# Kernel tuning notes

Hardware: AMD Instinct MI355X
Metric: run time of the kernel (lower is better)

## Reference

```python
import jax, jax.numpy as jnp
import numpy as np

K = 40  # neighbors, self.k = 40 in the module
BN_EPS = 1e-5


def knn(x, k):
    # x: (B, C, N) -> indices of k nearest points (largest negative sq-dist)
    xx = jnp.sum(x * x, axis=1, keepdims=True)            # (B, 1, N)
    inner = -2.0 * jnp.einsum('bcn,bcm->bnm', x, x)       # (B, N, N)
    pd = -xx - inner - jnp.swapaxes(xx, 1, 2)             # (B, N, N) = -||xi-xj||^2
    _, idx = jax.lax.top_k(pd, k)                         # (B, N, k)
    return idx


def graph_cov(x, k):
    # Faithful port of get_graph_dynamic_covariance (dim9=False, idx=None)
    B, C, N = x.shape
    idx = knn(x, k)                                       # (B, N, k)
    xt = jnp.swapaxes(x, 1, 2)                            # (B, N, C)
    feature = xt[jnp.arange(B)[:, None, None], idx]       # gather: (B, N, k, C)
    xc = xt[:, :, None, :]                                # (B, N, 1, C)
    rel = feature - xc                                    # relative positions
    var = jnp.var(rel, axis=2, ddof=1)                    # torch.var is unbiased
    relf = rel * (1.0 - var)[:, :, None, :]
    relf = jnp.concatenate([jnp.broadcast_to(xc, rel.shape), relf], axis=3)
    norm = rel - jnp.mean(rel, axis=0)                    # mean over BATCH dim, as in source
    cov = jnp.einsum('bnkc,bnjc->bnkj', rel, norm)        # (B, N, k, k)
    out = jnp.concatenate([relf, cov], axis=3)            # (B, N, k, 2C+k)
    return jnp.transpose(out, (0, 3, 1, 2))               # (B, 2C+k, N, k)


def bn(x, g, b):
    # train-mode BatchNorm (batch statistics, biased variance), eps=1e-5
    axes = (0,) + tuple(range(2, x.ndim))
    m = jnp.mean(x, axis=axes, keepdims=True)
    v = jnp.var(x, axis=axes, keepdims=True)
    shp = (1, -1) + (1,) * (x.ndim - 2)
    return g.reshape(shp) * (x - m) * jax.lax.rsqrt(v + BN_EPS) + b.reshape(shp)


def blk(x, W, g, b):
    # Conv(1x1, no bias) + BN + LeakyReLU(0.2)
    return jax.nn.leaky_relu(bn(jnp.einsum('oi,bi...->bo...', W, x), g, b), 0.2)


def forward(x, l, W3, W4, W5, W6, W7, W8, W9, W10, W11, W12,
            g3, b3, g4, b4, g5, b5, g6, b6, g7, b7, g8, b8, g9, b9,
            g10, b10, g11, b11):
    B, _, N = x.shape
    rc = blk(blk(graph_cov(x, K), W3, g3, b3), W4, g4, b4)       # (B,64,N,K)
    rc_ = jnp.max(rc, axis=-1)                                    # (B,64,N)
    drc = blk(blk(graph_cov(rc_, K), W5, g5, b5), W6, g6, b6)
    drc_ = jnp.max(drc, axis=-1)                                  # (B,64,N)
    allf = jnp.concatenate([rc_, drc_], axis=1)                   # (B,128,N)
    h = jnp.max(blk(allf, W7, g7, b7), axis=-1, keepdims=True)    # (B,1024,1)
    lv = blk(l.reshape(B, -1, 1), W8, g8, b8)                     # (B,64,1)
    h = jnp.concatenate([h, lv], axis=1)                          # (B,1088,1)
    h = jnp.broadcast_to(h, (B, h.shape[1], N))
    h = jnp.concatenate([h, rc_, drc_], axis=1)                   # (B,1216,N)
    h = blk(h, W9, g9, b9)
    h = blk(h, W10, g10, b10)                                     # dropout is eval-mode identity
    h = blk(h, W11, g11, b11)
    return jnp.einsum('oi,bin->bon', W12, h)                      # (B,50,N)


def setup_inputs():
    key = jax.random.key(0)
    ks = jax.random.split(key, 12)
    B, N = 4, 2048
    d = {}
    d['x'] = jax.random.normal(ks[0], (B, 3, N), jnp.float32)
    lab = jax.random.randint(ks[1], (B,), 0, 16)
    d['l'] = jax.nn.one_hot(lab, 16, dtype=jnp.float32)
    wdims = {'W3': (64, 46), 'W4': (64, 64), 'W5': (64, 168), 'W6': (64, 64),
             'W7': (1024, 128), 'W8': (64, 16), 'W9': (512, 1216),
             'W10': (256, 512), 'W11': (128, 256), 'W12': (50, 128)}
    for i, (name, shp) in enumerate(wdims.items()):
        d[name] = jax.random.normal(ks[2 + i], shp, jnp.float32) / np.float32(np.sqrt(shp[1]))
    for name, c in [('g3', 64), ('g4', 64), ('g5', 64), ('g6', 64), ('g7', 1024),
                    ('g8', 64), ('g9', 512), ('g10', 256), ('g11', 128)]:
        d[name] = jnp.ones((c,), jnp.float32)
        d['b' + name[1:]] = jnp.zeros((c,), jnp.float32)
    return d


def reference(x, l, W3, W4, W5, W6, W7, W8, W9, W10, W11, W12,
              g3, b3, g4, b4, g5, b5, g6, b6, g7, b7, g8, b8, g9, b9,
              g10, b10, g11, b11):
    return forward(x, l, W3, W4, W5, W6, W7, W8, W9, W10, W11, W12,
                   g3, b3, g4, b4, g5, b5, g6, b6, g7, b7, g8, b8, g9, b9,
                   g10, b10, g11, b11)
```

## Files before the change

### kernel.cpp

```cpp
#include <hip/hip_runtime.h>
#include <math.h>

#define NB 4
#define NP 2048
#define KNN 40
#define BEPS 1e-5f
#define NSLOT 64
#define CMCH 16

typedef unsigned long long u64;

static __device__ __forceinline__ float leaky(float x) { return x >= 0.f ? x : 0.2f * x; }

static __device__ __forceinline__ u64 keyOf(float v, int m) {
  unsigned u = __float_as_uint(v);
  u ^= (u >> 31) ? 0xFFFFFFFFu : 0x80000000u;
  return ((u64)u << 32) | (unsigned)(NP - 1 - m);
}
static __device__ __forceinline__ u64 umax64(u64 a, u64 b) { return a > b ? a : b; }

static __device__ __forceinline__ void select40_dual(float (*pd)[NP], int* __restrict__ out0,
                                                     int* __restrict__ out1, int tid,
                                                     u64* red, u64* red2, int* sh_w) {
  int h = tid >> 7, t = tid & 127;
  int* outp = h ? out1 : out0;
  u64 myBest = 0;
  #pragma unroll
  for (int j = 0; j < 16; ++j) myBest = umax64(myBest, keyOf(pd[h][t + j*128], t + j*128));
  for (int kk = 0; kk < KNN; ++kk) {
    red[tid] = myBest;
    __syncthreads();
    if (t < 16) {
      u64 v = red[h*128 + t];
      #pragma unroll
      for (int j = 1; j < 8; ++j) v = umax64(v, red[h*128 + t + j*16]);
      red2[h*16 + t] = v;
    }
    __syncthreads();
    if (t == 0) {
      u64 v = red2[h*16];
      #pragma unroll
      for (int j = 1; j < 16; ++j) v = umax64(v, red2[h*16 + j]);
      int w = NP - 1 - (int)(v & 0xFFFFFFFFu);
      outp[kk] = w;
      pd[h][w] = -INFINITY;
      sh_w[h] = w;
    }
    __syncthreads();
    if ((sh_w[h] & 127) == t) {
      u64 nb = 0;
      #pragma unroll
      for (int j = 0; j < 16; ++j) nb = umax64(nb, keyOf(pd[h][t + j*128], t + j*128));
      myBest = nb;
    }
  }
}

__global__ __launch_bounds__(256) void canary_kernel(float* __restrict__ out, int n, float val) {
  int i = blockIdx.x*256 + threadIdx.x;
  if (i < n) out[i] = val;
}

__global__ __launch_bounds__(256) void knn3_kernel(const float* __restrict__ x, int* __restrict__ idx) {
  int b = blockIdx.y, n0 = blockIdx.x*2, tid = threadIdx.x;
  __shared__ float pd[2][NP];
  __shared__ float xq[2][3];
  __shared__ float xxq[2];
  __shared__ u64 red[256];
  __shared__ u64 red2[32];
  __shared__ int sh_w[2];
  if (tid < 2) {
    int n = n0 + tid;
    float a0 = x[(b*3+0)*NP+n], a1 = x[(b*3+1)*NP+n], a2 = x[(b*3+2)*NP+n];
    xq[tid][0] = a0; xq[tid][1] = a1; xq[tid][2] = a2;
    xxq[tid] = __fadd_rn(__fadd_rn(__fmul_rn(a0,a0), __fmul_rn(a1,a1)), __fmul_rn(a2,a2));
  }
  __syncthreads();
  for (int m = tid; m < NP; m += 256) {
    float m0 = x[(b*3+0)*NP+m], m1 = x[(b*3+1)*NP+m], m2 = x[(b*3+2)*NP+m];
    float xxm = __fadd_rn(__fadd_rn(__fmul_rn(m0,m0), __fmul_rn(m1,m1)), __fmul_rn(m2,m2));
    #pragma unroll
    for (int q = 0; q < 2; ++q) {
      float dot = __fmaf_rn(xq[q][2], m2, __fmaf_rn(xq[q][1], m1, __fmul_rn(xq[q][0], m0)));
      float inner = __fmul_rn(-2.f, dot);
      pd[q][m] = __fsub_rn(__fsub_rn(-xxm, inner), xxq[q]);
    }
  }
  __syncthreads();
  select40_dual(pd, &idx[((size_t)b*NP + n0)*KNN], &idx[((size_t)b*NP + n0 + 1)*KNN], tid, red, red2, sh_w);
}

__global__ __launch_bounds__(256) void xx64_kernel(const float* __restrict__ rc, float* __restrict__ xx) {
  int i = blockIdx.x*256 + threadIdx.x;
  if (i >= NB*NP) return;
  const float* p = &rc[(size_t)i*64];
  float s = __fmul_rn(p[0], p[0]);
  #pragma unroll
  for (int c = 1; c < 64; ++c) s = __fadd_rn(s, __fmul_rn(p[c], p[c]));
  xx[i] = s;
}

__global__ __launch_bounds__(256) void knn64_kernel(const float* __restrict__ rc, const float* __restrict__ xx,
                                                    int* __restrict__ idx) {
  int b = blockIdx.y, n0 = blockIdx.x*2, tid = threadIdx.x;
  __shared__ float pd[2][NP];
  __shared__ float xn[2][64];
  __shared__ u64 red[256];
  __shared__ u64 red2[32];
  __shared__ int sh_w[2];
  if (tid < 128) xn[tid >> 6][tid & 63] = rc[((size_t)b*NP + n0 + (tid >> 6))*64 + (tid & 63)];
  __syncthreads();
  float xxn0 = xx[b*NP + n0], xxn1 = xx[b*NP + n0 + 1];
  for (int m = tid; m < NP; m += 256) {
    const float* xm = &rc[((size_t)b*NP + m)*64];
    float v0 = xm[0];
    float d0 = __fmul_rn(xn[0][0], v0);
    float d1 = __fmul_rn(xn[1][0], v0);
    #pragma unroll
    for (int c = 1; c < 64; ++c) {
      float v = xm[c];
      d0 = __fmaf_rn(xn[0][c], v, d0);
      d1 = __fmaf_rn(xn[1][c], v, d1);
    }
    float xxm = xx[b*NP + m];
    pd[0][m] = __fsub_rn(__fsub_rn(-xxm, __fmul_rn(-2.f, d0)), xxn0);
    pd[1][m] = __fsub_rn(__fsub_rn(-xxm, __fmul_rn(-2.f, d1)), xxn1);
  }
  __syncthreads();
  select40_dual(pd, &idx[((size_t)b*NP + n0)*KNN], &idx[((size_t)b*NP + n0 + 1)*KNN], tid, red, red2, sh_w);
}


__global__ __launch_bounds__(256) void s1a_kernel(
    const float* __restrict__ x, const int* __restrict__ idx1, const float* __restrict__ W3,
    double* __restrict__ stslots, float* __restrict__ y)
{
  int b = blockIdx.y, n = blockIdx.x, tid = threadIdx.x;
  __shared__ int sidx[4][KNN];
  __shared__ float rs[KNN][4];
  __shared__ float ns[KNN][4];
  __shared__ float scale[3];
  __shared__ __align__(16) float feat[KNN*48];
  __shared__ float w3s[64*48];
  __shared__ double sred[4][64];

  for (int i = tid; i < 4*KNN; i += 256) sidx[i/KNN][i%KNN] = idx1[((i/KNN)*NP + n)*KNN + (i%KNN)];
  for (int i = tid; i < 64*48; i += 256) { int o = i/48, ci = i%48; w3s[i] = (ci < 46) ? W3[o*46+ci] : 0.f; }
  __syncthreads();
  for (int i = tid; i < KNN*3; i += 256) {
    int k = i/3, c = i%3;
    float ctr = x[(b*3+c)*NP + n];
    float r = x[(b*3+c)*NP + sidx[b][k]] - ctr;
    float s = 0.f;
    for (int b2 = 0; b2 < 4; ++b2) s += x[(b2*3+c)*NP + sidx[b2][k]] - x[(b2*3+c)*NP + n];
    rs[k][c] = r; ns[k][c] = r - 0.25f*s;
  }
  __syncthreads();
  if (tid < 3) {
    float s = 0.f; for (int k = 0; k < KNN; ++k) s += rs[k][tid];
    float m = s/(float)KNN; float v = 0.f;
    for (int k = 0; k < KNN; ++k) { float d = rs[k][tid]-m; v += d*d; }
    scale[tid] = 1.f - v/(float)(KNN-1);
  }
  __syncthreads();
  for (int i = tid; i < KNN*48; i += 256) {
    int k = i/48, ci = i%48; float v;
    if (ci < 3) v = x[(b*3+ci)*NP+n];
    else if (ci < 6) v = rs[k][ci-3]*scale[ci-3];
    else if (ci < 46) { int j = ci-6; v = rs[k][0]*ns[j][0] + rs[k][1]*ns[j][1] + rs[k][2]*ns[j][2]; }
    else v = 0.f;
    feat[i] = v;
  }
  __syncthreads();

  int o = tid & 63, kg = tid >> 6;
  float acc[10];
  #pragma unroll
  for (int t = 0; t < 10; ++t) acc[t] = 0.f;
  for (int ci4 = 0; ci4 < 12; ++ci4) {
    float w0 = w3s[o*48+ci4*4+0], w1 = w3s[o*48+ci4*4+1], w2 = w3s[o*48+ci4*4+2], w3c = w3s[o*48+ci4*4+3];
    #pragma unroll
    for (int t = 0; t < 10; ++t) {
      float4 f4 = *(const float4*)&feat[(kg*10+t)*48 + ci4*4];
      acc[t] += f4.x*w0 + f4.y*w1 + f4.z*w2 + f4.w*w3c;
    }
  }
  size_t bn40 = (size_t)(b*NP+n)*KNN;
  #pragma unroll
  for (int t = 0; t < 10; ++t) y[(bn40 + kg*10+t)*64 + o] = acc[t];
  double s = 0.0, s2 = 0.0;
  #pragma unroll
  for (int t = 0; t < 10; ++t) { double a = acc[t]; s += a; s2 += a*a; }
  int slot = (blockIdx.y*NP + blockIdx.x) & (NSLOT-1);
  sred[kg][o] = s; __syncthreads();
  if (kg == 0) atomicAdd(&stslots[slot*128 + o], sred[0][o]+sred[1][o]+sred[2][o]+sred[3][o]);
  __syncthreads();
  sred[kg][o] = s2; __syncthreads();
  if (kg == 0) atomicAdd(&stslots[slot*128 + 64 + o], sred[0][o]+sred[1][o]+sred[2][o]+sred[3][o]);
}

__global__ __launch_bounds__(256) void s2a_kernel(
    const float* __restrict__ rc, const int* __restrict__ idx2, const float* __restrict__ W5,
    double* __restrict__ stslots, float* __restrict__ y)
{
  int b = blockIdx.y, n = blockIdx.x, tid = threadIdx.x;
  __shared__ int sidx[4][KNN];
  __shared__ float rsT[64*41];
  __shared__ float nsT[64*41];
  __shared__ float scale[64];
  __shared__ __align__(16) float feat[KNN*168];
  __shared__ double sred[4][64];

  for (int i = tid; i < 4*KNN; i += 256) sidx[i/KNN][i%KNN] = idx2[((i/KNN)*NP + n)*KNN + (i%KNN)];
  __syncthreads();
  for (int i = tid; i < KNN*64; i += 256) {
    int k = i >> 6, c = i & 63;
    float ctr = rc[((size_t)(b*NP+n))*64 + c];
    float r = rc[((size_t)(b*NP) + sidx[b][k])*64 + c] - ctr;
    float s = 0.f;
    for (int b2 = 0; b2 < 4; ++b2)
      s += rc[((size_t)(b2*NP) + sidx[b2][k])*64 + c] - rc[((size_t)(b2*NP+n))*64 + c];
    rsT[c*41+k] = r; nsT[c*41+k] = r - 0.25f*s;
  }
  __syncthreads();
  if (tid < 64) {
    int c = tid;
    float s = 0.f; for (int k = 0; k < KNN; ++k) s += rsT[c*41+k];
    float m = s/(float)KNN; float v = 0.f;
    for (int k = 0; k < KNN; ++k) { float d = rsT[c*41+k]-m; v += d*d; }
    scale[c] = 1.f - v/(float)(KNN-1);
  }
  __syncthreads();
  for (int i = tid; i < KNN*128; i += 256) {
    int k = i >> 7, ci = i & 127;
    float v;
    if (ci < 64) v = rc[((size_t)(b*NP+n))*64 + ci];
    else v = rsT[(ci-64)*41 + k]*scale[ci-64];
    feat[k*168 + ci] = v;
  }
  for (int p = tid; p < KNN*KNN; p += 256) {
    int k = p/KNN, j = p%KNN;
    float acc = __fmul_rn(rsT[k], nsT[j]);
    #pragma unroll 8
    for (int c = 1; c < 64; ++c) acc = __fmaf_rn(rsT[c*41+k], nsT[c*41+j], acc);
    feat[k*168 + 128 + j] = acc;
  }
  __syncthreads();

  int o = tid & 63, kg = tid >> 6;
  float acc[10];
  #pragma unroll
  for (int t = 0; t < 10; ++t) acc[t] = 0.f;
  for (int ci4 = 0; ci4 < 42; ++ci4) {
    float4 wv = *(const float4*)&W5[(size_t)o*168 + ci4*4];
    #pragma unroll
    for (int t = 0; t < 10; ++t) {
      float4 f4 = *(const float4*)&feat[(kg*10+t)*168 + ci4*4];
      acc[t] += f4.x*wv.x + f4.y*wv.y + f4.z*wv.z + f4.w*wv.w;
    }
  }
  size_t bn40 = (size_t)(b*NP+n)*KNN;
  #pragma unroll
  for (int t = 0; t < 10; ++t) y[(bn40 + kg*10+t)*64 + o] = acc[t];
  double s = 0.0, s2 = 0.0;
  #pragma unroll
  for (int t = 0; t < 10; ++t) { double a = acc[t]; s += a; s2 += a*a; }
  int slot = (blockIdx.y*NP + blockIdx.x) & (NSLOT-1);
  sred[kg][o] = s; __syncthreads();
  if (kg == 0) atomicAdd(&stslots[slot*128 + o], sred[0][o]+sred[1][o]+sred[2][o]+sred[3][o]);
  __syncthreads();
  sred[kg][o] = s2; __syncthreads();
  if (kg == 0) atomicAdd(&stslots[slot*128 + 64 + o], sred[0][o]+sred[1][o]+sred[2][o]+sred[3][o]);
}

__global__ __launch_bounds__(256) void mid_kernel(
    float* __restrict__ y, const float* __restrict__ W,
    const double* __restrict__ stp, const float* __restrict__ gv, const float* __restrict__ bv,
    double* __restrict__ stslots)
{
  int b = blockIdx.y, n = blockIdx.x, tid = threadIdx.x;
  __shared__ float m_s[64], sc_s[64], bo_s[64];
  __shared__ __align__(16) float ytile[KNN*68];
  __shared__ double sred[4][64];
  const double INV_M1 = 1.0/327680.0;

  if (tid < 64) {
    double md = stp[tid]*INV_M1;
    double vd = stp[64+tid]*INV_M1 - md*md;
    m_s[tid] = (float)md;
    sc_s[tid] = gv[tid]/sqrtf((float)vd + BEPS);
    bo_s[tid] = bv[tid];
  }
  __syncthreads();
  size_t bn40 = (size_t)(b*NP+n)*KNN;
  for (int i = tid; i < KNN*64; i += 256) {
    int k = i >> 6, c = i & 63;
    float v = y[(bn40 + k)*64 + c];
    ytile[k*68+c] = leaky(sc_s[c]*(v - m_s[c]) + bo_s[c]);
  }
  __syncthreads();
  int o = tid & 63, kg = tid >> 6;
  float acc2[10];
  #pragma unroll
  for (int t = 0; t < 10; ++t) acc2[t] = 0.f;
  for (int c4 = 0; c4 < 16; ++c4) {
    float4 wv = *(const float4*)&W[(size_t)o*64 + c4*4];
    #pragma unroll
    for (int t = 0; t < 10; ++t) {
      float4 y4 = *(const float4*)&ytile[(kg*10+t)*68 + c4*4];
      acc2[t] += y4.x*wv.x + y4.y*wv.y + y4.z*wv.z + y4.w*wv.w;
    }
  }
  #pragma unroll
  for (int t = 0; t < 10; ++t) y[(bn40 + kg*10+t)*64 + o] = acc2[t];
  double s = 0.0, s2 = 0.0;
  #pragma unroll
  for (int t = 0; t < 10; ++t) { double a = acc2[t]; s += a; s2 += a*a; }
  int slot = (blockIdx.y*NP + blockIdx.x) & (NSLOT-1);
  sred[kg][o] = s; __syncthreads();
  if (kg == 0) atomicAdd(&stslots[slot*128 + o], sred[0][o]+sred[1][o]+sred[2][o]+sred[3][o]);
  __syncthreads();
  sred[kg][o] = s2; __syncthreads();
  if (kg == 0) atomicAdd(&stslots[slot*128 + 64 + o], sred[0][o]+sred[1][o]+sred[2][o]+sred[3][o]);
}

__global__ __launch_bounds__(256) void maxk_bn_kernel(
    const float* __restrict__ y, const double* __restrict__ stp,
    const float* __restrict__ gv, const float* __restrict__ bv, float* __restrict__ out)
{
  int i = blockIdx.x*256 + threadIdx.x;
  if (i >= NB*NP*64) return;
  int o = i & 63; int bn = i >> 6;
  const double INV_M1 = 1.0/327680.0;
  double md = stp[o]*INV_M1;
  double vd = stp[64+o]*INV_M1 - md*md;
  float m = (float)md;
  float sc = gv[o]/sqrtf((float)vd + BEPS);
  float bo = bv[o];
  float mx = -INFINITY;
  size_t base = (size_t)bn*KNN;
  for (int k = 0; k < KNN; ++k) {
    float v = y[(base + k)*64 + o];
    mx = fmaxf(mx, leaky(sc*(v-m) + bo));
  }
  out[(size_t)bn*64 + o] = mx;
}

__global__ __launch_bounds__(128) void redstats_kernel(const double* __restrict__ slots, double* __restrict__ st) {
  int c = threadIdx.x;
  double s = 0.0;
  for (int i = 0; i < NSLOT; ++i) s += slots[i*128 + c];
  st[c] = s;
}

__global__ __launch_bounds__(256) void allf_kernel(const float* __restrict__ rc, const float* __restrict__ drc,
                                                   float* __restrict__ out) {
  int i = blockIdx.x*256 + threadIdx.x;
  if (i >= NB*NP*128) return;
  int c = i & 127; int bn = i >> 7;
  out[i] = (c < 64) ? rc[(size_t)bn*64 + c] : drc[(size_t)bn*64 + (c-64)];
}

#define GBM 64
#define GBN 64
#define GBK 16
__global__ __launch_bounds__(256) void gemm_kernel(const float* __restrict__ A, const float* __restrict__ W,
                                                   float* __restrict__ C, int M, int No, int Kd,
                                                   int wstride, int woff, const float* __restrict__ bias) {
  __shared__ __align__(16) float As[GBK][GBM+8];
  __shared__ __align__(16) float Ws[GBK][GBN+8];
  int bm = blockIdx.y * GBM, bn = blockIdx.x * GBN;
  int tid = threadIdx.x;
  int tx = tid % 16, ty = tid / 16;
  float acc[4][4] = {{0.f}};
  for (int k0 = 0; k0 < Kd; k0 += GBK) {
    for (int i = tid; i < GBM*GBK; i += 256) {
      int r = i / GBK, c = i % GBK;
      int gm = bm + r, gk = k0 + c;
      As[c][r] = (gk < Kd && gm < M) ? A[(size_t)gm*Kd + gk] : 0.f;
      int gn = bn + r;
      Ws[c][r] = (gk < Kd && gn < No) ? W[(size_t)gn*wstride + woff + gk] : 0.f;
    }
    __syncthreads();
    #pragma unroll
    for (int kk = 0; kk < GBK; ++kk) {
      float4 a4 = *(const float4*)&As[kk][ty*4];
      float4 w4 = *(const float4*)&Ws[kk][tx*4];
      float av[4] = {a4.x, a4.y, a4.z, a4.w};
      float wv[4] = {w4.x, w4.y, w4.z, w4.w};
      #pragma unroll
      for (int i2 = 0; i2 < 4; ++i2)
        #pragma unroll
        for (int j2 = 0; j2 < 4; ++j2)
          acc[i2][j2] += av[i2]*wv[j2];
    }
    __syncthreads();
  }
  for (int i2 = 0; i2 < 4; ++i2) {
    int gm = bm + ty*4 + i2;
    if (gm >= M) continue;
    for (int j2 = 0; j2 < 4; ++j2) {
      int gn = bn + tx*4 + j2;
      if (gn < No) {
        float v = acc[i2][j2];
        if (bias) v += bias[(gm >> 11)*No + gn];
        C[(size_t)gm*No + gn] = v;
      }
    }
  }
}

__global__ __launch_bounds__(256) void colstats_kernel(const float* __restrict__ A, long M, int C,
                                                       int rowsPerBlock, double* __restrict__ st) {
  long r0 = (long)blockIdx.x * rowsPerBlock;
  long r1 = r0 + rowsPerBlock; if (r1 > M) r1 = M;
  int tid = threadIdx.x;
  if (C >= 256) {
    for (int c0 = 0; c0 < C; c0 += 256) {
      int c = c0 + tid;
      double s = 0.0, s2 = 0.0;
      for (long r = r0; r < r1; ++r) { double v = A[r*(long)C + c]; s += v; s2 += v*v; }
      atomicAdd(&st[c], s); atomicAdd(&st[C+c], s2);
    }
  } else {
    int c = tid % C; int grp = tid / C; int G = 256 / C;
    double s = 0.0, s2 = 0.0;
    for (long r = r0 + grp; r < r1; r += G) { double v = A[r*(long)C + c]; s += v; s2 += v*v; }
    __shared__ double sh[512];
    sh[tid] = s; sh[256+tid] = s2; __syncthreads();
    for (int g = G/2; g > 0; g >>= 1) {
      if (grp < g) { sh[tid] += sh[tid + g*C]; sh[256+tid] += sh[256+tid + g*C]; }
      __syncthreads();
    }
    if (grp == 0) { atomicAdd(&st[c], sh[tid]); atomicAdd(&st[C+c], sh[256+tid]); }
  }
}

__global__ __launch_bounds__(256) void bnapply_kernel(float* __restrict__ A, const double* __restrict__ st,
                                                      const float* __restrict__ g, const float* __restrict__ bb,
                                                      double invM, int cmask, size_t total) {
  size_t i = (size_t)blockIdx.x*256 + threadIdx.x;
  if (i >= total) return;
  int c = (int)(i & cmask);
  int C = cmask + 1;
  double md = st[c]*invM;
  double vd = st[C+c]*invM - md*md;
  float m = (float)md;
  float sc = g[c]/sqrtf((float)vd + BEPS);
  float y = sc*(A[i]-m) + bb[c];
  A[i] = leaky(y);
}

__global__ __launch_bounds__(256) void colmax_part_kernel(const float* __restrict__ A, int C,
                                                          float* __restrict__ pmax) {
  int i = blockIdx.x*256 + threadIdx.x;
  if (i >= NB*CMCH*C) return;
  int c = i % C; int t = i / C; int ch = t % CMCH; int b = t / CMCH;
  int n0 = ch * (NP/CMCH);
  float mx = -INFINITY;
  for (int n = n0; n < n0 + NP/CMCH; ++n)
    mx = fmaxf(mx, A[((size_t)(b*NP+n))*C + c]);
  pmax[(size_t)(b*CMCH+ch)*C + c] = mx;
}
__global__ __launch_bounds__(256) void colmax_fin_kernel(const float* __restrict__ pmax, int C,
                                                         float* __restrict__ out) {
  int i = blockIdx.x*256 + threadIdx.x;
  if (i >= NB*C) return;
  int b = i / C, c = i % C;
  float mx = -INFINITY;
  for (int ch = 0; ch < CMCH; ++ch) mx = fmaxf(mx, pmax[(size_t)(b*CMCH+ch)*C + c]);
  out[i] = mx;
}

__global__ __launch_bounds__(256) void lv_kernel(const float* __restrict__ l, const float* __restrict__ W8,
                                                 const float* __restrict__ g8, const float* __restrict__ b8,
                                                 float* __restrict__ lv) {
  __shared__ float raw[4][64];
  int tid = threadIdx.x;
  {
    int b = tid / 64, o = tid % 64;
    float s = 0.f;
    for (int i = 0; i < 16; ++i) s += W8[o*16+i]*l[b*16+i];
    raw[b][o] = s;
  }
  __syncthreads();
  if (tid < 64) {
    int o = tid;
    float m = (raw[0][o]+raw[1][o]+raw[2][o]+raw[3][o])*0.25f;
    float v = 0.f;
    for (int b = 0; b < 4; ++b) { float d = raw[b][o]-m; v += d*d; }
    v *= 0.25f;
    float sc = g8[o]/sqrtf(v + BEPS);
    for (int b = 0; b < 4; ++b) {
      float y = sc*(raw[b][o]-m) + b8[o];
      lv[b*64+o] = leaky(y);
    }
  }
}

__global__ __launch_bounds__(256) void bias9_kernel(const float* __restrict__ hmax, const float* __restrict__ lv,
                                                    const float* __restrict__ W9, float* __restrict__ bias9) {
  int i = blockIdx.x*256 + threadIdx.x;
  if (i >= 4*512) return;
  int b = i >> 9, o = i & 511;
  const float* wr = &W9[(size_t)o*1216];
  float s = 0.f;
  for (int c = 0; c < 1024; ++c) s += hmax[b*1024+c]*wr[c];
  for (int c = 0; c < 64; ++c) s += lv[b*64+c]*wr[1024+c];
  bias9[i] = s;
}

__global__ __launch_bounds__(256) void out_kernel(const float* __restrict__ h5, float* __restrict__ out) {
  int i = blockIdx.x*256 + threadIdx.x;
  if (i >= NB*50*NP) return;
  int n = i % NP; int t = i / NP; int o = t % 50; int b = t / 50;
  out[i] = h5[((size_t)(b*NP+n))*50 + o];
}

extern "C" void kernel_launch(void* const* d_in, const int* in_sizes, int n_in,
                              void* d_out, int out_size, void* d_ws, size_t ws_size,
                              hipStream_t stream) {
  const float* x   = (const float*)d_in[0];
  const float* l   = (const float*)d_in[1];
  const float* W3  = (const float*)d_in[2];
  const float* W4  = (const float*)d_in[3];
  const float* W5  = (const float*)d_in[4];
  const float* W6  = (const float*)d_in[5];
  const float* W7  = (const float*)d_in[6];
  const float* W8  = (const float*)d_in[7];
  const float* W9  = (const float*)d_in[8];
  const float* W10 = (const float*)d_in[9];
  const float* W11 = (const float*)d_in[10];
  const float* W12 = (const float*)d_in[11];
  const float* g3 = (const float*)d_in[12], *b3 = (const float*)d_in[13];
  const float* g4 = (const float*)d_in[14], *b4 = (const float*)d_in[15];
  const float* g5 = (const float*)d_in[16], *b5 = (const float*)d_in[17];
  const float* g6 = (const float*)d_in[18], *b6 = (const float*)d_in[19];
  const float* g7 = (const float*)d_in[20], *b7 = (const float*)d_in[21];
  const float* g8 = (const float*)d_in[22], *b8 = (const float*)d_in[23];
  const float* g9 = (const float*)d_in[24], *b9 = (const float*)d_in[25];
  const float* g10 = (const float*)d_in[26], *b10 = (const float*)d_in[27];
  const float* g11 = (const float*)d_in[28], *b11 = (const float*)d_in[29];
  (void)in_sizes; (void)n_in;

  constexpr size_t OFF_IDX1 = 0;
  constexpr size_t OFF_IDX2 = OFF_IDX1 + (size_t)NB*NP*KNN*4;
  constexpr size_t OFF_RC   = OFF_IDX2 + (size_t)NB*NP*KNN*4;
  constexpr size_t OFF_DRC  = OFF_RC   + (size_t)NB*NP*64*4;
  constexpr size_t OFF_XX   = OFF_DRC  + (size_t)NB*NP*64*4;
  constexpr size_t OFF_SLOT = OFF_XX   + (size_t)NB*NP*4;
  constexpr size_t OFF_ST3  = OFF_SLOT + (size_t)NSLOT*128*8;
  constexpr size_t OFF_ST4  = OFF_ST3 + 128*8;
  constexpr size_t OFF_ST5  = OFF_ST4 + 128*8;
  constexpr size_t OFF_ST6  = OFF_ST5 + 128*8;
  constexpr size_t OFF_STH  = OFF_ST6 + 128*8;
  constexpr size_t OFF_HMAX = OFF_STH + 2*1024*8;
  constexpr size_t OFF_LV   = OFF_HMAX + 4*1024*4;
  constexpr size_t OFF_B9   = OFF_LV + 4096;
  constexpr size_t OFF_PMAX = OFF_B9 + 4*512*4;
  constexpr size_t OFF_ALLF = OFF_PMAX + (size_t)NB*CMCH*1024*4;
  constexpr size_t OFF_H1   = OFF_ALLF + (size_t)NB*NP*128*4;
  constexpr size_t SZ_H1    = (size_t)NB*NP*1024*4;
  constexpr size_t OFF_END  = OFF_H1 + SZ_H1;
  constexpr size_t OFF_H2 = OFF_H1;
  constexpr size_t OFF_H3 = OFF_H2 + (size_t)NB*NP*512*4;
  constexpr size_t OFF_H4 = OFF_H3 + (size_t)NB*NP*256*4;
  constexpr size_t OFF_H5 = OFF_H4 + (size_t)NB*NP*128*4;
  static_assert(OFF_H5 + (size_t)NB*NP*50*4 <= OFF_END, "h alias overflow");
  constexpr size_t OFF_Y   = OFF_END;
  constexpr size_t SZ_Y    = (size_t)NB*NP*KNN*64*4;
  constexpr size_t OFF_FAST_END = OFF_Y + SZ_Y;

  if (ws_size < OFF_END) {
    canary_kernel<<<(out_size + 255)/256, 256, 0, stream>>>((float*)d_out, out_size, (float)(ws_size >> 20));
    return;
  }
  const bool FAST = (ws_size >= OFF_FAST_END);

  char* ws = (char*)d_ws;
  int*    idx1  = (int*)(ws + OFF_IDX1);
  int*    idx2  = (int*)(ws + OFF_IDX2);
  float*  rc    = (float*)(ws + OFF_RC);
  float*  drc   = (float*)(ws + OFF_DRC);
  float*  xx2   = (float*)(ws + OFF_XX);
  double* slots = (double*)(ws + OFF_SLOT);
  double* st3s  = (double*)(ws + OFF_ST3);
  double* st4s  = (double*)(ws + OFF_ST4);
  double* st5s  = (double*)(ws + OFF_ST5);
  double* st6s  = (double*)(ws + OFF_ST6);
  double* sth   = (double*)(ws + OFF_STH);
  float*  hmaxb = (float*)(ws + OFF_HMAX);
  float*  lvb   = (float*)(ws + OFF_LV);
  float*  bias9 = (float*)(ws + OFF_B9);
  float*  pmaxb = (float*)(ws + OFF_PMAX);
  float*  allf  = (float*)(ws + OFF_ALLF);
  float*  h1    = (float*)(ws + OFF_H1);
  float*  h2    = (float*)(ws + OFF_H2);
  float*  h3    = (float*)(ws + OFF_H3);
  float*  h4    = (float*)(ws + OFF_H4);
  float*  h5    = (float*)(ws + OFF_H5);
  float*  ybuf  = (float*)(ws + OFF_Y);

  dim3 gridNP(NP, NB);
  dim3 gridKNN2(NP/2, NB);
  const size_t slotBytes = (size_t)NSLOT*128*8;
  const double INV_M2 = 1.0/8192.0;

  knn3_kernel<<<gridKNN2, 256, 0, stream>>>(x, idx1);
  hipMemsetAsync(slots, 0, slotBytes, stream);
  s1a_kernel<<<gridNP, 256, 0, stream>>>(x, idx1, W3, slots, FAST ? ybuf : h1);
  redstats_kernel<<<1, 128, 0, stream>>>(slots, st3s);
  hipMemsetAsync(slots, 0, slotBytes, stream);
  mid_kernel<<<gridNP, 256, 0, stream>>>(FAST ? ybuf : h1, W4, st3s, g3, b3, slots);
  redstats_kernel<<<1, 128, 0, stream>>>(slots, st4s);
  maxk_bn_kernel<<<(NB*NP*64 + 255)/256, 256, 0, stream>>>(FAST ? ybuf : h1, st4s, g4, b4, rc);

  xx64_kernel<<<(NB*NP + 255)/256, 256, 0, stream>>>(rc, xx2);
  knn64_kernel<<<gridKNN2, 256, 0, stream>>>(rc, xx2, idx2);
  hipMemsetAsync(slots, 0, slotBytes, stream);
  s2a_kernel<<<gridNP, 256, 0, stream>>>(rc, idx2, W5, slots, FAST ? ybuf : h1);
  redstats_kernel<<<1, 128, 0, stream>>>(slots, st5s);
  hipMemsetAsync(slots, 0, slotBytes, stream);
  mid_kernel<<<gridNP, 256, 0, stream>>>(FAST ? ybuf : h1, W6, st5s, g5, b5, slots);
  redstats_kernel<<<1, 128, 0, stream>>>(slots, st6s);
  maxk_bn_kernel<<<(NB*NP*64 + 255)/256, 256, 0, stream>>>(FAST ? ybuf : h1, st6s, g6, b6, drc);

  allf_kernel<<<(NB*NP*128 + 255)/256, 256, 0, stream>>>(rc, drc, allf);
  gemm_kernel<<<dim3(1024/GBN, 8192/GBM), 256, 0, stream>>>(allf, W7, h1, 8192, 1024, 128, 128, 0, nullptr);
  hipMemsetAsync(sth, 0, 2*1024*8, stream);
  colstats_kernel<<<128, 256, 0, stream>>>(h1, 8192, 1024, 64, sth);
  bnapply_kernel<<<(unsigned)(((size_t)8192*1024 + 255)/256), 256, 0, stream>>>(h1, sth, g7, b7, INV_M2, 1023, (size_t)8192*1024);
  colmax_part_kernel<<<(NB*CMCH*1024 + 255)/256, 256, 0, stream>>>(h1, 1024, pmaxb);
  colmax_fin_kernel<<<(NB*1024 + 255)/256, 256, 0, stream>>>(pmaxb, 1024, hmaxb);
  lv_kernel<<<1, 256, 0, stream>>>(l, W8, g8, b8, lvb);
  bias9_kernel<<<8, 256, 0, stream>>>(hmaxb, lvb, W9, bias9);

  gemm_kernel<<<dim3(512/GBN, 8192/GBM), 256, 0, stream>>>(allf, W9, h2, 8192, 512, 128, 1216, 1088, bias9);
  hipMemsetAsync(sth, 0, 2*512*8, stream);
  colstats_kernel<<<128, 256, 0, stream>>>(h2, 8192, 512, 64, sth);
  bnapply_kernel<<<(unsigned)(((size_t)8192*512 + 255)/256), 256, 0, stream>>>(h2, sth, g9, b9, INV_M2, 511, (size_t)8192*512);

  gemm_kernel<<<dim3(256/GBN, 8192/GBM), 256, 0, stream>>>(h2, W10, h3, 8192, 256, 512, 512, 0, nullptr);
  hipMemsetAsync(sth, 0, 2*256*8, stream);
  colstats_kernel<<<128, 256, 0, stream>>>(h3, 8192, 256, 64, sth);
  bnapply_kernel<<<(unsigned)(((size_t)8192*256 + 255)/256), 256, 0, stream>>>(h3, sth, g10, b10, INV_M2, 255, (size_t)8192*256);

  gemm_kernel<<<dim3(128/GBN, 8192/GBM), 256, 0, stream>>>(h3, W11, h4, 8192, 128, 256, 256, 0, nullptr);
  hipMemsetAsync(sth, 0, 2*128*8, stream);
  colstats_kernel<<<128, 256, 0, stream>>>(h4, 8192, 128, 64, sth);
  bnapply_kernel<<<(unsigned)(((size_t)8192*128 + 255)/256), 256, 0, stream>>>(h4, sth, g11, b11, INV_M2, 127, (size_t)8192*128);

  gemm_kernel<<<dim3(1, 8192/GBM), 256, 0, stream>>>(h4, W12, h5, 8192, 50, 128, 128, 0, nullptr);
  out_kernel<<<(NB*50*NP + 255)/256, 256, 0, stream>>>(h5, (float*)d_out);
}
```

Before: 1.523 ms.

## Fold covariance block into W5 weights to skip building the 40x40 covariance feature

The per-point stage no longer materialises the 40x168 feature matrix in shared memory, including the 40x40 covariance block. Because conv(W5) over the covariance is linear, W5's covariance columns are first contracted with the normalized relative features, and the variance scale is folded in, giving a 64x64 matrix u. The output is then computed as rsT times u plus a per-point center term. This replaces roughly 40*40*64 plus 40*64*168 multiply-adds with about 64*64*40 plus 40*64*64, and shrinks shared memory use, at the cost of a changed floating-point summation order.

```diff
diff --git a/kernel.cpp b/kernel.cpp
--- a/kernel.cpp
+++ b/kernel.cpp
@@ -208,7 +208,8 @@
   __shared__ float rsT[64*41];
   __shared__ float nsT[64*41];
   __shared__ float scale[64];
-  __shared__ __align__(16) float feat[KNN*168];
+  __shared__ float u[64*65];
+  __shared__ float acc0s[64];
   __shared__ double sred[4][64];
 
   for (int i = tid; i < 4*KNN; i += 256) sidx[i/KNN][i%KNN] = idx2[((i/KNN)*NP + n)*KNN + (i%KNN)];
@@ -231,33 +232,33 @@
     scale[c] = 1.f - v/(float)(KNN-1);
   }
   __syncthreads();
-  for (int i = tid; i < KNN*128; i += 256) {
-    int k = i >> 7, ci = i & 127;
-    float v;
-    if (ci < 64) v = rc[((size_t)(b*NP+n))*64 + ci];
-    else v = rsT[(ci-64)*41 + k]*scale[ci-64];
-    feat[k*168 + ci] = v;
-  }
-  for (int p = tid; p < KNN*KNN; p += 256) {
-    int k = p/KNN, j = p%KNN;
-    float acc = __fmul_rn(rsT[k], nsT[j]);
+  for (int i = tid; i < 64*64; i += 256) {
+    int o = i >> 6, c = i & 63;
+    const float* wr = &W5[(size_t)o*168];
+    float a = __fmul_rn(wr[64+c], scale[c]);
     #pragma unroll 8
-    for (int c = 1; c < 64; ++c) acc = __fmaf_rn(rsT[c*41+k], nsT[c*41+j], acc);
-    feat[k*168 + 128 + j] = acc;
+    for (int j = 0; j < KNN; ++j) a = __fmaf_rn(wr[128+j], nsT[c*41+j], a);
+    u[o*65+c] = a;
+  }
+  if (tid < 64) {
+    int o = tid;
+    const float* wr = &W5[(size_t)o*168];
+    const float* xc = &rc[((size_t)(b*NP+n))*64];
+    float a = 0.f;
+    for (int c = 0; c < 64; ++c) a = __fmaf_rn(wr[c], xc[c], a);
+    acc0s[o] = a;
   }
   __syncthreads();
 
   int o = tid & 63, kg = tid >> 6;
   float acc[10];
   #pragma unroll
-  for (int t = 0; t < 10; ++t) acc[t] = 0.f;
-  for (int ci4 = 0; ci4 < 42; ++ci4) {
-    float4 wv = *(const float4*)&W5[(size_t)o*168 + ci4*4];
+  for (int t = 0; t < 10; ++t) acc[t] = acc0s[o];
+  for (int c = 0; c < 64; ++c) {
+    float uoc = u[o*65+c];
+    const float* rsc = &rsT[c*41 + kg*10];
     #pragma unroll
-    for (int t = 0; t < 10; ++t) {
-      float4 f4 = *(const float4*)&feat[(kg*10+t)*168 + ci4*4];
-      acc[t] += f4.x*wv.x + f4.y*wv.y + f4.z*wv.z + f4.w*wv.w;
-    }
+    for (int t = 0; t < 10; ++t) acc[t] = __fmaf_rn(rsc[t], uoc, acc[t]);
   }
   size_t bn40 = (size_t)(b*NP+n)*KNN;
   #pragma unroll
```

After: 1.480 ms, median of 3. 2.8% less time.
